# Kernel optimization log

Measured on AMD Instinct MI355X. Metric: run time of the kernel, lower is better.

## Reference

```python
import jax, jax.numpy as jnp
import numpy as np

B, T, H, D, V = 1, 512, 12, 64, 32000  # batch, seq, heads, head_dim, vocab


def setup_inputs() -> dict:
    key = jax.random.key(0)
    k0, k1, k2, k3 = jax.random.split(key, 4)
    x = jax.random.normal(k0, (B, T, H * D), dtype=jnp.float32)
    # per-head FFN weights: torch Linear(head_dim, head_dim) -> weight (out,in)=(D,D)
    W_ffn = jax.random.normal(k1, (H, D, D), dtype=jnp.float32) * 0.02
    b_ffn = jnp.zeros((H, D), dtype=jnp.float32)
    # per-head vocab attention: torch Linear(head_dim, vocab_size, bias=False) -> weight (V,D)
    W_vocab = jax.random.normal(k2, (H, V, D), dtype=jnp.float32) * 0.02
    temps = jnp.ones((H,), dtype=jnp.float32)
    # shared vocab embedding table (vocab_size, n_embd)
    E = jax.random.normal(k3, (V, H * D), dtype=jnp.float32) * 0.02
    return {"x": x, "W_ffn": W_ffn, "b_ffn": b_ffn, "W_vocab": W_vocab,
            "temps": temps, "E": E}


def reference(x, W_ffn, b_ffn, W_vocab, temps, E):
    Bx, Tx, C = x.shape
    Hn, Dn, _ = W_ffn.shape
    xh = x.reshape(Bx, Tx, Hn, Dn)                         # (B,T,H,D)
    # per-head FFN (Linear: y = x @ W^T + b)
    ffn = jnp.einsum('bthd,hed->bthe', xh, W_ffn) + b_ffn  # (B,T,H,D)
    # per-head vocab logits against weight bank (H,V,D)
    logits = jnp.einsum('bthd,hvd->bthv', ffn, W_vocab)    # (B,T,H,V)
    temp = jnp.maximum(temps, 0.1)[None, None, :, None]    # clamp(min=0.1)
    w = jax.nn.softmax(logits / temp, axis=-1)             # (B,T,H,V)
    # back-project through per-head slices of vocab embedding table
    Eh = E.reshape(E.shape[0], Hn, Dn)                     # (V,H,D)
    out = jnp.einsum('bthv,vhd->bthd', w, Eh)              # (B,T,H,D)
    # dropout is identity at eval (p used at train only)
    return out.reshape(Bx, Tx, C)
```

## Files before the change

### kernel.cpp

```cpp
#include <hip/hip_runtime.h>
#include <hip/hip_bf16.h>
#include <cstddef>

#define T_TOK 512
#define NH    12
#define HD    64
#define NV    32000
#define CEMB  768
#define NC    20
#define VC    (NV/NC)
#define NSUB  (VC/64)
#define QTILE 256
#define LOG2E 1.44269504088896340736f

typedef short v8bf __attribute__((ext_vector_type(8)));
typedef float v4f  __attribute__((ext_vector_type(4)));

__device__ __forceinline__ unsigned short f2bf(float f) {
    unsigned u = __float_as_uint(f);
    u += 0x7fffu + ((u >> 16) & 1u);
    return (unsigned short)(u >> 16);
}
__device__ __forceinline__ unsigned cvtpk(float a, float b) {
    unsigned r;
    asm("v_cvt_pk_bf16_f32 %0, %1, %2" : "=v"(r) : "v"(a), "v"(b));
    return r;
}
__device__ __forceinline__ float bf2f(unsigned short u) {
    return __uint_as_float(((unsigned)u) << 16);
}
__device__ __forceinline__ void gld16(const void* g, void* l) {
    __builtin_amdgcn_global_load_lds(
        (const __attribute__((address_space(1))) unsigned*)g,
        (__attribute__((address_space(3))) unsigned*)l, 16, 0, 0);
}

__global__ __launch_bounds__(256) void ffn_kernel(
        const float* __restrict__ x, const float* __restrict__ Wf,
        const float* __restrict__ bf, const float* __restrict__ temps,
        unsigned short* __restrict__ Qb) {
    const int h = blockIdx.y;
    const int tl = threadIdx.x >> 6, e = threadIdx.x & 63;
    const int t = blockIdx.x * 4 + tl;
    __shared__ float xs[4][HD];
    xs[tl][e] = x[t*CEMB + h*HD + e];
    __syncthreads();
    const float4* w4  = (const float4*)(Wf + (size_t)(h*HD + e)*HD);
    const float4* xs4 = (const float4*)xs[tl];
    float acc = bf[h*HD + e];
    #pragma unroll
    for (int i = 0; i < HD/4; ++i) {
        float4 a = xs4[i], b = w4[i];
        acc += a.x*b.x + a.y*b.y + a.z*b.z + a.w*b.w;
    }
    float tau = temps[h]; tau = (tau < 0.1f) ? 0.1f : tau;
    Qb[((size_t)h*T_TOK + t)*HD + e] = f2bf(acc * LOG2E / tau);
}

__global__ __launch_bounds__(256) void e_transpose(const float* __restrict__ E,
                                                   unsigned short* __restrict__ ET) {
    const int v0 = blockIdx.x * 64, h = blockIdx.y;
    const int tid = threadIdx.x;
    __shared__ float Ts[64*65];
    #pragma unroll
    for (int r = 0; r < 4; ++r) {
        int f = tid + 256*r, v = f >> 4, d4 = f & 15;
        float4 e4 = *(const float4*)&E[(size_t)(v0 + v)*CEMB + h*HD + d4*4];
        Ts[(d4*4+0)*65 + v] = e4.x;
        Ts[(d4*4+1)*65 + v] = e4.y;
        Ts[(d4*4+2)*65 + v] = e4.z;
        Ts[(d4*4+3)*65 + v] = e4.w;
    }
    __syncthreads();
    #pragma unroll
    for (int r = 0; r < 2; ++r) {
        int u = tid + 256*r, d = u >> 3, c16 = u & 7;
        const float* row = &Ts[d*65 + c16*8];
        uint4 w;
        w.x = cvtpk(row[0], row[1]);
        w.y = cvtpk(row[2], row[3]);
        w.z = cvtpk(row[4], row[5]);
        w.w = cvtpk(row[6], row[7]);
        *(uint4*)&ET[(size_t)(h*64 + d)*NV + v0 + c16*8] = w;
    }
}

__global__ __launch_bounds__(256, 2) void flash_mfma(
        const unsigned short* __restrict__ Qb, const float* __restrict__ Wv,
        const unsigned short* __restrict__ ET, unsigned short* __restrict__ Npart,
        float* __restrict__ Zpart) {
    const int g    = blockIdx.x;
    const int xcd  = g & 7, slot = g >> 3;
    const int qg   = slot & 1;
    const int p    = (slot >> 1)*8 + xcd;
    const int c    = p % NC;
    const int h    = p / NC;

    const int tid  = threadIdx.x;
    const int wq   = tid >> 6;
    const int lane = tid & 63;
    const int l15  = lane & 15, quad = lane >> 4;
    const int X    = l15 & 7;

    __shared__ unsigned short Kb[2][64*64];
    __shared__ unsigned short Eb[2][64*64];
    __shared__ unsigned short Ps[QTILE*64];

    const int tbase = qg*QTILE + wq*64;

    v8bf qf[4][2];
    #pragma unroll
    for (int nt = 0; nt < 4; ++nt)
        #pragma unroll
        for (int kb = 0; kb < 2; ++kb)
            qf[nt][kb] = *(const v8bf*)&Qb[((size_t)h*T_TOK + tbase + nt*16 + l15)*HD
                                           + kb*32 + quad*8];

    v4f o[4][4];
    #pragma unroll
    for (int mt = 0; mt < 4; ++mt)
        #pragma unroll
        for (int nt = 0; nt < 4; ++nt) { v4f z = {0.f,0.f,0.f,0.f}; o[mt][nt] = z; }
    float zacc[4] = {0.f, 0.f, 0.f, 0.f};

    const int kv = wq*16 + (lane >> 2);
    const int Xk = kv & 7;
    const float* kgl = Wv + ((size_t)h*NV + (size_t)c*VC + kv)*HD + (lane & 3)*4;
    int kwoff[4];
    #pragma unroll
    for (int r = 0; r < 4; ++r)
        kwoff[r] = kv*64 + (((((lane&3)>>1) + 2*r) ^ Xk))*8 + (lane&1)*4;
    const int Gv = (lane & 7) ^ (lane >> 3);
    const unsigned short* eg0 = ET + (size_t)(h*64 + wq*16 + (lane >> 3))*NV
                                   + (size_t)c*VC + Gv*8;
    const unsigned short* eg1 = eg0 + (size_t)8*NV;

    {
        gld16(eg0, &Eb[0][(wq*16)*64]);
        gld16(eg1, &Eb[0][(wq*16 + 8)*64]);
        float4 k0[4];
        #pragma unroll
        for (int r = 0; r < 4; ++r) k0[r] = *(const float4*)(kgl + r*16);
        #pragma unroll
        for (int r = 0; r < 4; ++r) {
            uint2 w = { cvtpk(k0[r].x, k0[r].y), cvtpk(k0[r].z, k0[r].w) };
            *(uint2*)&Kb[0][kwoff[r]] = w;
        }
        __syncthreads();
    }

    int nb = 1;
    for (int s = 0; s < NSUB; ++s) {
        const int cur = nb ^ 1;
        const bool pre = (s + 1 < NSUB);
        float4 kr[4];
        if (pre) {
            gld16(eg0 + (s+1)*64, &Eb[nb][(wq*16)*64]);
            gld16(eg1 + (s+1)*64, &Eb[nb][(wq*16 + 8)*64]);
            #pragma unroll
            for (int r = 0; r < 4; ++r)
                kr[r] = *(const float4*)(kgl + (size_t)(s+1)*4096 + r*16);
        }

        v8bf kf[4][2];
        #pragma unroll
        for (int mt = 0; mt < 4; ++mt) {
            const int row = (mt*16 + l15)*64;
            kf[mt][0] = *(const v8bf*)&Kb[cur][row + ((quad     ^ X))*8];
            kf[mt][1] = *(const v8bf*)&Kb[cur][row + (((4+quad) ^ X))*8];
        }
        #pragma unroll
        for (int nt = 0; nt < 4; ++nt) {
            #pragma unroll
            for (int mt = 0; mt < 4; ++mt) {
                v4f sa = {0.f,0.f,0.f,0.f};
                sa = __builtin_amdgcn_mfma_f32_16x16x32_bf16(kf[mt][0], qf[nt][0], sa, 0, 0, 0);
                sa = __builtin_amdgcn_mfma_f32_16x16x32_bf16(kf[mt][1], qf[nt][1], sa, 0, 0, 0);
                float p0 = exp2f(sa[0]), p1 = exp2f(sa[1]);
                float p2 = exp2f(sa[2]), p3 = exp2f(sa[3]);
                zacc[nt] += (p0 + p1) + (p2 + p3);
                uint2 w = { cvtpk(p0, p1), cvtpk(p2, p3) };
                const int q = wq*64 + nt*16 + l15;
                *(uint2*)&Ps[q*64 + (((mt*2 + (quad>>1)) ^ X))*8 + (quad&1)*4] = w;
            }
        }

        v8bf ef[4][2];
        #pragma unroll
        for (int mt = 0; mt < 4; ++mt) {
            const int row = (mt*16 + l15)*64;
            ef[mt][0] = *(const v8bf*)&Eb[cur][row + ((quad     ^ X))*8];
            ef[mt][1] = *(const v8bf*)&Eb[cur][row + (((4+quad) ^ X))*8];
        }
        #pragma unroll
        for (int nt = 0; nt < 4; ++nt) {
            const int q = wq*64 + nt*16 + l15;
            v8bf pf0 = *(const v8bf*)&Ps[q*64 + ((quad     ^ X))*8];
            v8bf pf1 = *(const v8bf*)&Ps[q*64 + (((4+quad) ^ X))*8];
            #pragma unroll
            for (int mt = 0; mt < 4; ++mt) {
                o[mt][nt] = __builtin_amdgcn_mfma_f32_16x16x32_bf16(ef[mt][0], pf0, o[mt][nt], 0, 0, 0);
                o[mt][nt] = __builtin_amdgcn_mfma_f32_16x16x32_bf16(ef[mt][1], pf1, o[mt][nt], 0, 0, 0);
            }
        }

        if (pre) {
            #pragma unroll
            for (int r = 0; r < 4; ++r) {
                uint2 w = { cvtpk(kr[r].x, kr[r].y), cvtpk(kr[r].z, kr[r].w) };
                *(uint2*)&Kb[nb][kwoff[r]] = w;
            }
            __syncthreads();
        }
        nb ^= 1;
    }

    #pragma unroll
    for (int nt = 0; nt < 4; ++nt) {
        float z = zacc[nt];
        z += __shfl_xor(z, 16, 64);
        z += __shfl_xor(z, 32, 64);
        if (quad == 0)
            Zpart[((size_t)c*T_TOK + tbase + nt*16 + l15)*NH + h] = z;
    }
    #pragma unroll
    for (int nt = 0; nt < 4; ++nt) {
        const int t = tbase + nt*16 + l15;
        unsigned short* np = Npart + (((size_t)c*T_TOK + t)*NH + h)*HD;
        #pragma unroll
        for (int mt = 0; mt < 4; ++mt) {
            v4f ov = o[mt][nt];
            uint2 w = { cvtpk(ov[0], ov[1]), cvtpk(ov[2], ov[3]) };
            *(uint2*)&np[mt*16 + quad*4] = w;
        }
    }
}

__global__ void combine_kernel(const unsigned short* __restrict__ Npart,
                               const float* __restrict__ Zpart,
                               float* __restrict__ out) {
    const int idx = (blockIdx.x*256 + threadIdx.x)*4;
    const int t = idx / CEMB;
    const int rem = idx % CEMB;
    const int h = rem >> 6, d = rem & 63;
    float n0 = 0.f, n1 = 0.f, n2 = 0.f, n3 = 0.f, z = 0.f;
    #pragma unroll
    for (int c = 0; c < NC; ++c) {
        uint2 u = *(const uint2*)&Npart[(((size_t)c*T_TOK + t)*NH + h)*HD + d];
        n0 += bf2f((unsigned short)(u.x & 0xffffu));
        n1 += bf2f((unsigned short)(u.x >> 16));
        n2 += bf2f((unsigned short)(u.y & 0xffffu));
        n3 += bf2f((unsigned short)(u.y >> 16));
        z  += Zpart[((size_t)c*T_TOK + t)*NH + h];
    }
    const float rz = 1.0f / z;
    float4 o = { n0*rz, n1*rz, n2*rz, n3*rz };
    *(float4*)&out[idx] = o;
}

extern "C" void kernel_launch(void* const* d_in, const int* in_sizes, int n_in,
                              void* d_out, int out_size, void* d_ws, size_t ws_size,
                              hipStream_t stream) {
    const float* x     = (const float*)d_in[0];
    const float* Wf    = (const float*)d_in[1];
    const float* bf    = (const float*)d_in[2];
    const float* Wv    = (const float*)d_in[3];
    const float* temps = (const float*)d_in[4];
    const float* E     = (const float*)d_in[5];
    float* out = (float*)d_out;

    char* ws = (char*)d_ws;
    unsigned short* Npart = (unsigned short*)ws;
    float*          Zpart = (float*)(ws + 15728640);
    unsigned short* Qb    = (unsigned short*)(ws + 16220160);
    unsigned short* ET    = (unsigned short*)(ws + 17006592);

    e_transpose   <<<dim3(NV/64, NH),         256, 0, stream>>>(E, ET);
    ffn_kernel    <<<dim3(T_TOK/4, NH),       256, 0, stream>>>(x, Wf, bf, temps, Qb);
    flash_mfma    <<<dim3(NC*2*NH),           256, 0, stream>>>(Qb, Wv, ET, Npart, Zpart);
    combine_kernel<<<dim3((T_TOK*CEMB)/1024), 256, 0, stream>>>(Npart, Zpart, out);
}
```

Before: 314.1 us.

## Switch flash kernel to 32x32x16 MFMA and keep probabilities in registers

The main attention kernel now uses 32x32x16 bf16 MFMA tiles instead of 16x16x32. The exponentiated scores are rearranged into B-operand layout with v_permlane32_swap, so they no longer round-trip through the Ps shared-memory buffer. Blocks grow to 512 threads (8 waves of 32 tokens each) with launch bounds of 4 per CU, and the K/E staging loads are reshaped to fit. This removes LDS traffic and the Ps allocation and raises waves per CU. The cost is higher register pressure from the 16-wide accumulators and reliance on exact lane-layout correctness of the permlane swap.

```diff
diff --git a/kernel.cpp b/kernel.cpp
--- a/kernel.cpp
+++ b/kernel.cpp
@@ -13,8 +13,9 @@
 #define QTILE 256
 #define LOG2E 1.44269504088896340736f
 
-typedef short v8bf __attribute__((ext_vector_type(8)));
-typedef float v4f  __attribute__((ext_vector_type(4)));
+typedef short v8bf  __attribute__((ext_vector_type(8)));
+typedef float v16f  __attribute__((ext_vector_type(16)));
+typedef unsigned uv4 __attribute__((ext_vector_type(4)));
 
 __device__ __forceinline__ unsigned short f2bf(float f) {
     unsigned u = __float_as_uint(f);
@@ -25,6 +26,9 @@
     unsigned r;
     asm("v_cvt_pk_bf16_f32 %0, %1, %2" : "=v"(r) : "v"(a), "v"(b));
     return r;
+}
+__device__ __forceinline__ void pl32swap(unsigned &x, unsigned &y) {
+    asm("v_permlane32_swap_b32 %0, %1" : "+v"(x), "+v"(y));
 }
 __device__ __forceinline__ float bf2f(unsigned short u) {
     return __uint_as_float(((unsigned)u) << 16);
@@ -85,7 +89,7 @@
     }
 }
 
-__global__ __launch_bounds__(256, 2) void flash_mfma(
+__global__ __launch_bounds__(512, 4) void flash_mfma(
         const unsigned short* __restrict__ Qb, const float* __restrict__ Wv,
         const unsigned short* __restrict__ ET, unsigned short* __restrict__ Npart,
         float* __restrict__ Zpart) {
@@ -99,53 +103,36 @@
     const int tid  = threadIdx.x;
     const int wq   = tid >> 6;
     const int lane = tid & 63;
-    const int l15  = lane & 15, quad = lane >> 4;
-    const int X    = l15 & 7;
+    const int l31  = lane & 31, hi = lane >> 5;
 
     __shared__ unsigned short Kb[2][64*64];
     __shared__ unsigned short Eb[2][64*64];
-    __shared__ unsigned short Ps[QTILE*64];
-
-    const int tbase = qg*QTILE + wq*64;
-
-    v8bf qf[4][2];
-    #pragma unroll
-    for (int nt = 0; nt < 4; ++nt)
-        #pragma unroll
-        for (int kb = 0; kb < 2; ++kb)
-            qf[nt][kb] = *(const v8bf*)&Qb[((size_t)h*T_TOK + tbase + nt*16 + l15)*HD
-                                           + kb*32 + quad*8];
-
-    v4f o[4][4];
-    #pragma unroll
-    for (int mt = 0; mt < 4; ++mt)
-        #pragma unroll
-        for (int nt = 0; nt < 4; ++nt) { v4f z = {0.f,0.f,0.f,0.f}; o[mt][nt] = z; }
-    float zacc[4] = {0.f, 0.f, 0.f, 0.f};
-
-    const int kv = wq*16 + (lane >> 2);
-    const int Xk = kv & 7;
-    const float* kgl = Wv + ((size_t)h*NV + (size_t)c*VC + kv)*HD + (lane & 3)*4;
-    int kwoff[4];
-    #pragma unroll
-    for (int r = 0; r < 4; ++r)
-        kwoff[r] = kv*64 + (((((lane&3)>>1) + 2*r) ^ Xk))*8 + (lane&1)*4;
-    const int Gv = (lane & 7) ^ (lane >> 3);
-    const unsigned short* eg0 = ET + (size_t)(h*64 + wq*16 + (lane >> 3))*NV
-                                   + (size_t)c*VC + Gv*8;
-    const unsigned short* eg1 = eg0 + (size_t)8*NV;
+
+    const int tbase = qg*QTILE + wq*32;
+
+    v8bf qf[4];
+    #pragma unroll
+    for (int k16 = 0; k16 < 4; ++k16)
+        qf[k16] = *(const v8bf*)&Qb[((size_t)h*T_TOK + tbase + l31)*HD
+                                    + k16*16 + hi*8];
+
+    v16f o0, o1;
+    #pragma unroll
+    for (int r = 0; r < 16; ++r) { o0[r] = 0.f; o1[r] = 0.f; }
+    float zacc = 0.f;
+
+    const int kv = wq*8 + (lane >> 3);
+    const float* kgl = Wv + ((size_t)h*NV + (size_t)c*VC + kv)*HD + (lane & 7)*8;
+    const int kwoff = kv*64 + (((lane & 7) ^ (lane >> 3)))*8;
+    const unsigned short* eg = ET + (size_t)(h*64 + wq*8 + (lane >> 3))*NV
+                                  + (size_t)c*VC + (((lane & 7) ^ (lane >> 3)))*8;
 
     {
-        gld16(eg0, &Eb[0][(wq*16)*64]);
-        gld16(eg1, &Eb[0][(wq*16 + 8)*64]);
-        float4 k0[4];
-        #pragma unroll
-        for (int r = 0; r < 4; ++r) k0[r] = *(const float4*)(kgl + r*16);
-        #pragma unroll
-        for (int r = 0; r < 4; ++r) {
-            uint2 w = { cvtpk(k0[r].x, k0[r].y), cvtpk(k0[r].z, k0[r].w) };
-            *(uint2*)&Kb[0][kwoff[r]] = w;
-        }
+        gld16(eg, &Eb[0][(wq*8)*64]);
+        float4 a = *(const float4*)(kgl);
+        float4 b = *(const float4*)(kgl + 4);
+        uv4 w = { cvtpk(a.x,a.y), cvtpk(a.z,a.w), cvtpk(b.x,b.y), cvtpk(b.z,b.w) };
+        *(uv4*)&Kb[0][kwoff] = w;
         __syncthreads();
     }
 
@@ -153,85 +140,86 @@
     for (int s = 0; s < NSUB; ++s) {
         const int cur = nb ^ 1;
         const bool pre = (s + 1 < NSUB);
-        float4 kr[4];
+        float4 ka, kb2;
         if (pre) {
-            gld16(eg0 + (s+1)*64, &Eb[nb][(wq*16)*64]);
-            gld16(eg1 + (s+1)*64, &Eb[nb][(wq*16 + 8)*64]);
-            #pragma unroll
-            for (int r = 0; r < 4; ++r)
-                kr[r] = *(const float4*)(kgl + (size_t)(s+1)*4096 + r*16);
-        }
-
-        v8bf kf[4][2];
+            gld16(eg + (s+1)*64, &Eb[nb][(wq*8)*64]);
+            ka  = *(const float4*)(kgl + (size_t)(s+1)*4096);
+            kb2 = *(const float4*)(kgl + (size_t)(s+1)*4096 + 4);
+        }
+
+        uv4 pfw[4];
         #pragma unroll
-        for (int mt = 0; mt < 4; ++mt) {
-            const int row = (mt*16 + l15)*64;
-            kf[mt][0] = *(const v8bf*)&Kb[cur][row + ((quad     ^ X))*8];
-            kf[mt][1] = *(const v8bf*)&Kb[cur][row + (((4+quad) ^ X))*8];
-        }
+        for (int vt = 0; vt < 2; ++vt) {
+            v8bf kf[4];
+            #pragma unroll
+            for (int k16 = 0; k16 < 4; ++k16) {
+                const int row = vt*32 + l31;
+                kf[k16] = *(const v8bf*)&Kb[cur][row*64 + ((k16*2 + hi) ^ (row & 7))*8];
+            }
+            v16f sa;
+            #pragma unroll
+            for (int r = 0; r < 16; ++r) sa[r] = 0.f;
+            #pragma unroll
+            for (int k16 = 0; k16 < 4; ++k16)
+                sa = __builtin_amdgcn_mfma_f32_32x32x16_bf16(kf[k16], qf[k16], sa, 0, 0, 0);
+            unsigned W[8];
+            #pragma unroll
+            for (int gi = 0; gi < 4; ++gi) {
+                float pa = exp2f(sa[4*gi+0]), pb = exp2f(sa[4*gi+1]);
+                float pc = exp2f(sa[4*gi+2]), pd = exp2f(sa[4*gi+3]);
+                zacc += (pa + pb) + (pc + pd);
+                W[2*gi+0] = cvtpk(pa, pb);
+                W[2*gi+1] = cvtpk(pc, pd);
+            }
+            unsigned x0 = W[0], y0 = W[2];  pl32swap(x0, y0);
+            unsigned x1 = W[1], y1 = W[3];  pl32swap(x1, y1);
+            pfw[vt*2 + 0] = (uv4){ x0, x1, y0, y1 };
+            unsigned x2 = W[4], y2 = W[6];  pl32swap(x2, y2);
+            unsigned x3 = W[5], y3 = W[7];  pl32swap(x3, y3);
+            pfw[vt*2 + 1] = (uv4){ x2, x3, y2, y3 };
+        }
+
         #pragma unroll
-        for (int nt = 0; nt < 4; ++nt) {
-            #pragma unroll
-            for (int mt = 0; mt < 4; ++mt) {
-                v4f sa = {0.f,0.f,0.f,0.f};
-                sa = __builtin_amdgcn_mfma_f32_16x16x32_bf16(kf[mt][0], qf[nt][0], sa, 0, 0, 0);
-                sa = __builtin_amdgcn_mfma_f32_16x16x32_bf16(kf[mt][1], qf[nt][1], sa, 0, 0, 0);
-                float p0 = exp2f(sa[0]), p1 = exp2f(sa[1]);
-                float p2 = exp2f(sa[2]), p3 = exp2f(sa[3]);
-                zacc[nt] += (p0 + p1) + (p2 + p3);
-                uint2 w = { cvtpk(p0, p1), cvtpk(p2, p3) };
-                const int q = wq*64 + nt*16 + l15;
-                *(uint2*)&Ps[q*64 + (((mt*2 + (quad>>1)) ^ X))*8 + (quad&1)*4] = w;
-            }
-        }
-
-        v8bf ef[4][2];
-        #pragma unroll
-        for (int mt = 0; mt < 4; ++mt) {
-            const int row = (mt*16 + l15)*64;
-            ef[mt][0] = *(const v8bf*)&Eb[cur][row + ((quad     ^ X))*8];
-            ef[mt][1] = *(const v8bf*)&Eb[cur][row + (((4+quad) ^ X))*8];
-        }
-        #pragma unroll
-        for (int nt = 0; nt < 4; ++nt) {
-            const int q = wq*64 + nt*16 + l15;
-            v8bf pf0 = *(const v8bf*)&Ps[q*64 + ((quad     ^ X))*8];
-            v8bf pf1 = *(const v8bf*)&Ps[q*64 + (((4+quad) ^ X))*8];
-            #pragma unroll
-            for (int mt = 0; mt < 4; ++mt) {
-                o[mt][nt] = __builtin_amdgcn_mfma_f32_16x16x32_bf16(ef[mt][0], pf0, o[mt][nt], 0, 0, 0);
-                o[mt][nt] = __builtin_amdgcn_mfma_f32_16x16x32_bf16(ef[mt][1], pf1, o[mt][nt], 0, 0, 0);
-            }
+        for (int dt = 0; dt < 2; ++dt) {
+            v8bf ef[4];
+            #pragma unroll
+            for (int k16 = 0; k16 < 4; ++k16) {
+                const int row = dt*32 + l31;
+                ef[k16] = *(const v8bf*)&Eb[cur][row*64 + ((k16*2 + hi) ^ (row & 7))*8];
+            }
+            v16f oo = dt ? o1 : o0;
+            #pragma unroll
+            for (int k16 = 0; k16 < 4; ++k16)
+                oo = __builtin_amdgcn_mfma_f32_32x32x16_bf16(
+                        ef[k16], __builtin_bit_cast(v8bf, pfw[k16]), oo, 0, 0, 0);
+            if (dt) o1 = oo; else o0 = oo;
         }
 
         if (pre) {
-            #pragma unroll
-            for (int r = 0; r < 4; ++r) {
-                uint2 w = { cvtpk(kr[r].x, kr[r].y), cvtpk(kr[r].z, kr[r].w) };
-                *(uint2*)&Kb[nb][kwoff[r]] = w;
-            }
+            uv4 w = { cvtpk(ka.x,ka.y), cvtpk(ka.z,ka.w),
+                      cvtpk(kb2.x,kb2.y), cvtpk(kb2.z,kb2.w) };
+            *(uv4*)&Kb[nb][kwoff] = w;
             __syncthreads();
         }
         nb ^= 1;
     }
 
-    #pragma unroll
-    for (int nt = 0; nt < 4; ++nt) {
-        float z = zacc[nt];
-        z += __shfl_xor(z, 16, 64);
-        z += __shfl_xor(z, 32, 64);
-        if (quad == 0)
-            Zpart[((size_t)c*T_TOK + tbase + nt*16 + l15)*NH + h] = z;
-    }
-    #pragma unroll
-    for (int nt = 0; nt < 4; ++nt) {
-        const int t = tbase + nt*16 + l15;
+    zacc += __shfl_xor(zacc, 32, 64);
+    if (hi == 0)
+        Zpart[((size_t)c*T_TOK + tbase + l31)*NH + h] = zacc;
+
+    {
+        const int t = tbase + l31;
         unsigned short* np = Npart + (((size_t)c*T_TOK + t)*NH + h)*HD;
         #pragma unroll
-        for (int mt = 0; mt < 4; ++mt) {
-            v4f ov = o[mt][nt];
-            uint2 w = { cvtpk(ov[0], ov[1]), cvtpk(ov[2], ov[3]) };
-            *(uint2*)&np[mt*16 + quad*4] = w;
+        for (int dt = 0; dt < 2; ++dt) {
+            v16f oo = dt ? o1 : o0;
+            #pragma unroll
+            for (int gi = 0; gi < 4; ++gi) {
+                uint2 w = { cvtpk(oo[4*gi+0], oo[4*gi+1]),
+                            cvtpk(oo[4*gi+2], oo[4*gi+3]) };
+                *(uint2*)&np[dt*32 + gi*8 + hi*4] = w;
+            }
         }
     }
 }
@@ -277,6 +265,6 @@
 
     e_transpose   <<<dim3(NV/64, NH),         256, 0, stream>>>(E, ET);
     ffn_kernel    <<<dim3(T_TOK/4, NH),       256, 0, stream>>>(x, Wf, bf, temps, Qb);
-    flash_mfma    <<<dim3(NC*2*NH),           256, 0, stream>>>(Qb, Wv, ET, Npart, Zpart);
+    flash_mfma    <<<dim3(NC*2*NH),           512, 0, stream>>>(Qb, Wv, ET, Npart, Zpart);
     combine_kernel<<<dim3((T_TOK*CEMB)/1024), 256, 0, stream>>>(Npart, Zpart, out);
 }
```

After: 299.8 us. 4.5% less time.
